# Performance work log

Measured on AMD Instinct MI355X. Metric: run time of the kernel, lower is better.

## Reference

```python
import jax, jax.numpy as jnp
import numpy as np

LEAK = 0.5  # LeakyReLU negative slope


def _binarize(w):
    # sign binarization with straight-through estimator (standard BinarizeConv2d /
    # CIM-sim quantized-weight behavior): forward uses sign(w) in {-1,+1},
    # backward passes gradient straight through.
    wb = jnp.where(w >= 0, 1.0, -1.0).astype(w.dtype)
    return w + jax.lax.stop_gradient(wb - w)


def _conv(x, w, b):
    # NCHW / OIHW, stride 1, no padding (matches nn.Conv2d(k, stride=1) defaults)
    y = jax.lax.conv_general_dilated(
        x, _binarize(w), window_strides=(1, 1), padding='VALID',
        dimension_numbers=('NCHW', 'OIHW', 'NCHW'))
    return y + b[None, :, None, None]


def _leaky(x):
    return jnp.where(x >= 0, x, LEAK * x)


def _maxpool2(x):
    # MaxPool2d(kernel_size=2), stride 2, floor mode == VALID reduce_window
    return jax.lax.reduce_window(x, -jnp.inf, jax.lax.max,
                                 (1, 1, 2, 2), (1, 1, 2, 2), 'VALID')


def setup_inputs() -> dict:
    key = jax.random.key(0)
    ks = jax.random.split(key, 9)
    f32 = jnp.float32
    return {
        'x':  jax.random.normal(ks[0], (32, 1, 224, 224), f32),
        'w1': jax.random.normal(ks[1], (128, 1, 3, 3), f32) * 0.1,
        'b1': jax.random.normal(ks[2], (128,), f32) * 0.1,
        'w2': jax.random.normal(ks[3], (64, 128, 3, 3), f32) * 0.1,
        'b2': jax.random.normal(ks[4], (64,), f32) * 0.1,
        'w3': jax.random.normal(ks[5], (32, 64, 3, 3), f32) * 0.1,
        'b3': jax.random.normal(ks[6], (32,), f32) * 0.1,
        'w4': jax.random.normal(ks[7], (8, 32, 3, 2), f32) * 0.1,
        'b4': jax.random.normal(ks[8], (8,), f32) * 0.1,
    }


def reference(x, w1, b1, w2, b2, w3, b3, w4, b4):
    x = _maxpool2(_leaky(_conv(x, w1, b1)))   # [B,128,111,111]
    x = _maxpool2(_leaky(_conv(x, w2, b2)))   # [B,64,54,54]
    x = _maxpool2(_leaky(_conv(x, w3, b3)))   # [B,32,26,26]
    x = _conv(x, w4, b4)                       # [B,8,24,25]
    return x.reshape(x.shape[0], -1)           # [B,4800]
```

## Files before the change

### kernel.cpp

```cpp
#include <hip/hip_runtime.h>
#include <hip/hip_bf16.h>

using bf16 = __hip_bfloat16;
typedef short  short8  __attribute__((ext_vector_type(8)));
typedef float  f32x4   __attribute__((ext_vector_type(4)));
typedef float  f32x16  __attribute__((ext_vector_type(16)));
typedef unsigned short us4 __attribute__((ext_vector_type(4)));

static __device__ __forceinline__ bf16  f2b(float v) { return __float2bfloat16(v); }
static __device__ __forceinline__ unsigned short f2bu(float v) {
    bf16 t = __float2bfloat16(v);
    return *(unsigned short*)&t;
}

__device__ __forceinline__ void pack32_one(const float* __restrict__ w,
                                           bf16* __restrict__ o, int i, int IC) {
    int j = i & 7;
    int l = (i >> 3) & 63;
    int f = i >> 9;
    int ICD16 = IC >> 4;
    int cc = f % ICD16;
    int t  = f / ICD16;
    int r  = t % 9;
    int mt = t / 9;
    int oc = mt * 32 + (l & 31);
    int ic = cc * 16 + ((l >> 5) << 3) + j;
    o[i] = f2b((w[(oc * IC + ic) * 9 + r] >= 0.f) ? 1.f : -1.f);
}

__global__ __launch_bounds__(256) void binpack_kernel(
    const float* __restrict__ w1, const float* __restrict__ w2,
    const float* __restrict__ w3, const float* __restrict__ w4,
    bf16* __restrict__ w1m, bf16* __restrict__ wA2,
    bf16* __restrict__ wA3, float* __restrict__ wc4) {
    int i = blockIdx.x * 256 + threadIdx.x;
    if (i < 73728) {
        pack32_one(w2, wA2, i, 128);
    } else if (i < 73728 + 18432) {
        pack32_one(w3, wA3, i - 73728, 64);
    } else if (i < 73728 + 18432 + 2048) {
        int k = i - (73728 + 18432);
        int j = k & 7, l = (k >> 3) & 63, mt = k >> 9;
        int ch = mt * 32 + (l & 31);
        int t = ((l >> 5) << 3) + j;
        w1m[k] = f2b(t < 9 ? ((w1[ch * 9 + t] >= 0.f) ? 1.f : -1.f) : 0.f);
    } else if (i < 73728 + 18432 + 2048 + 1536) {
        int k = i - (73728 + 18432 + 2048);
        int oc = k / 192, rem = k % 192;
        int ic = rem / 6, r = rem % 6;
        wc4[oc * 192 + r * 32 + ic] = (w4[k] >= 0.f) ? 1.f : -1.f;
    }
}

__global__ __launch_bounds__(256, 4) void conv1_kernel(
    const float* __restrict__ x, const bf16* __restrict__ w1m,
    const float* __restrict__ b1, bf16* __restrict__ a1) {
    __shared__ float xt[10][20];
    const int tid = threadIdx.x;
    const int b = blockIdx.z;
    const int pw0 = blockIdx.x * 8;
    const int ph0 = blockIdx.y * 4;
    const int r0 = ph0 * 2;
    const int c0 = pw0 * 2;

    if (tid < 180) {
        int row = tid / 18, col = tid - row * 18;
        int gr = r0 + row, gc = c0 + col;
        xt[row][col] = (gr < 224 && gc < 224)
                           ? x[((size_t)b * 224 + gr) * 224 + gc] : 0.f;
    }
    __syncthreads();

    const int w  = tid >> 6;
    const int l  = tid & 63;
    const int lc = l & 15;
    const int r2 = (l >> 4) & 1;
    const int hh = l >> 5;

    short8 af[4];
#pragma unroll
    for (int mt = 0; mt < 4; ++mt)
        af[mt] = ((const short8*)w1m)[mt * 64 + l];

    const int hl = 2 * w + r2;
    short8 bf;
    if (hh == 0) {
        bf[0] = (short)f2bu(xt[hl + 0][lc + 0]);
        bf[1] = (short)f2bu(xt[hl + 0][lc + 1]);
        bf[2] = (short)f2bu(xt[hl + 0][lc + 2]);
        bf[3] = (short)f2bu(xt[hl + 1][lc + 0]);
        bf[4] = (short)f2bu(xt[hl + 1][lc + 1]);
        bf[5] = (short)f2bu(xt[hl + 1][lc + 2]);
        bf[6] = (short)f2bu(xt[hl + 2][lc + 0]);
        bf[7] = (short)f2bu(xt[hl + 2][lc + 1]);
    } else {
        bf[0] = (short)f2bu(xt[hl + 2][lc + 2]);
        bf[1] = 0; bf[2] = 0; bf[3] = 0;
        bf[4] = 0; bf[5] = 0; bf[6] = 0; bf[7] = 0;
    }

    f32x16 acc[4];
#pragma unroll
    for (int mt = 0; mt < 4; ++mt) {
#pragma unroll
        for (int q = 0; q < 16; ++q) acc[mt][q] = 0.f;
        acc[mt] = __builtin_amdgcn_mfma_f32_32x32x16_bf16(af[mt], bf, acc[mt],
                                                          0, 0, 0);
    }

    const bool wr = ((l & 17) == 0);
    const int pw = pw0 + (lc >> 1);
    const int ph = ph0 + w;
    if (ph < 111 && pw < 111) {
#pragma unroll
        for (int mt = 0; mt < 4; ++mt) {
#pragma unroll
            for (int g = 0; g < 4; ++g) {
                f32x4 bias = *(const f32x4*)(b1 + mt * 32 + 8 * g + 4 * hh);
                us4 o;
#pragma unroll
                for (int q2 = 0; q2 < 4; ++q2) {
                    float v = acc[mt][g * 4 + q2] + bias[q2];
                    v = (v >= 0.f) ? v : 0.5f * v;
                    float m1 = fmaxf(v, __shfl_xor(v, 1));
                    float m  = fmaxf(m1, __shfl_xor(m1, 16));
                    o[q2] = f2bu(m);
                }
                if (wr)
                    *(us4*)(&a1[((size_t)(b * 111 + ph) * 111 + pw) * 128 +
                                mt * 32 + 8 * g + 4 * hh]) = o;
            }
        }
    }
}

template <int IC, int OC, int IN, int POOL>
__global__ __launch_bounds__(256, 4) void convmfma_kernel(
    const bf16* __restrict__ in, const bf16* __restrict__ wAp,
    const float* __restrict__ bias, bf16* __restrict__ out) {
    constexpr int MT = OC / 32;
    constexpr int CHUNKS = IC / 32;
    constexpr int ICD16 = IC / 16;
    __shared__ __align__(16) char smem[18 * 18 * 64];

    const int tid = threadIdx.x;
    const int b = blockIdx.z;
    const int oh0 = blockIdx.y * 16;
    const int ow0 = blockIdx.x * 16;

    const int w   = tid >> 6;
    const int l   = tid & 63;
    const int lc4 = l & 15;
    const int r2  = (l >> 4) & 1;
    const int hh  = l >> 5;

    f32x16 acc[MT][2];
#pragma unroll
    for (int mt = 0; mt < MT; ++mt)
#pragma unroll
        for (int nt = 0; nt < 2; ++nt)
#pragma unroll
            for (int q = 0; q < 16; ++q) acc[mt][nt][q] = 0.f;

    for (int chunk = 0; chunk < CHUNKS; ++chunk) {
        if (chunk) __syncthreads();
        {
            const bf16* src = in + ((size_t)b * IN * IN) * IC + chunk * 32;
            for (int u = tid; u < 18 * 18 * 4; u += 256) {
                int slot = u & 3, cell = u >> 2;
                int row = cell / 18, col = cell - row * 18;
                int gr = oh0 + row, gc = ow0 + col;
                f32x4 v = {0.f, 0.f, 0.f, 0.f};
                if (gr < IN && gc < IN)
                    v = *(const f32x4*)(src + ((size_t)gr * IN + gc) * IC + slot * 8);
                *(f32x4*)(smem + cell * 64 + ((slot ^ ((col >> 1) & 3)) << 4)) = v;
            }
        }
        __syncthreads();

#pragma unroll
        for (int kh = 0; kh < 3; ++kh) {
#pragma unroll
            for (int kw = 0; kw < 3; ++kw) {
                const int r = kh * 3 + kw;
                const int wincol = lc4 + kw;
                const int sx = (wincol >> 1) & 3;
#pragma unroll
                for (int cc = 0; cc < 2; ++cc) {
                    short8 af[MT];
#pragma unroll
                    for (int mt = 0; mt < MT; ++mt)
                        af[mt] = ((const short8*)wAp)[
                            (((mt * 9 + r) * ICD16) + chunk * 2 + cc) * 64 + l];
                    const int slot = cc * 2 + hh;
                    short8 bfr[2];
#pragma unroll
                    for (int nt = 0; nt < 2; ++nt) {
                        int cell = (4 * w + 2 * nt + r2 + kh) * 18 + wincol;
                        bfr[nt] = *(const short8*)(
                            smem + cell * 64 + ((slot ^ sx) << 4));
                    }
#pragma unroll
                    for (int mt = 0; mt < MT; ++mt)
#pragma unroll
                        for (int nt = 0; nt < 2; ++nt)
                            acc[mt][nt] = __builtin_amdgcn_mfma_f32_32x32x16_bf16(
                                af[mt], bfr[nt], acc[mt][nt], 0, 0, 0);
                }
            }
        }
    }

    const bool wr = ((l & 17) == 0);
    const int pw = blockIdx.x * 8 + (lc4 >> 1);
#pragma unroll
    for (int mt = 0; mt < MT; ++mt) {
#pragma unroll
        for (int nt = 0; nt < 2; ++nt) {
            const int ph = blockIdx.y * 8 + 2 * w + nt;
#pragma unroll
            for (int g = 0; g < 4; ++g) {
                us4 o;
#pragma unroll
                for (int q2 = 0; q2 < 4; ++q2) {
                    int q = g * 4 + q2;
                    int oc = mt * 32 + 8 * g + 4 * hh + q2;
                    float v = acc[mt][nt][q] + bias[oc];
                    v = (v >= 0.f) ? v : 0.5f * v;
                    float m1 = fmaxf(v, __shfl_xor(v, 1));
                    float m  = fmaxf(m1, __shfl_xor(m1, 16));
                    o[q2] = f2bu(m);
                }
                if (wr && ph < POOL && pw < POOL)
                    *(us4*)(&out[((size_t)(b * POOL + ph) * POOL + pw) * OC +
                                 mt * 32 + 8 * g + 4 * hh]) = o;
            }
        }
    }
}

__global__ __launch_bounds__(256) void conv4_kernel(
    const bf16* __restrict__ a3, const float* __restrict__ wc4,
    const float* __restrict__ b4, float* __restrict__ out) {
    int i = blockIdx.x * 256 + threadIdx.x;
    if (i >= 32 * 4800) return;
    int b = i / 4800;
    int rem = i % 4800;
    int oc = rem / 600;
    int r2 = rem % 600;
    int oh = r2 / 25, ow = r2 % 25;

    float acc = b4[oc];
    int rr = 0;
#pragma unroll
    for (int kh = 0; kh < 3; ++kh) {
#pragma unroll
        for (int kw = 0; kw < 2; ++kw, ++rr) {
            const bf16* xp = a3 + ((size_t)(b * 26 + oh + kh) * 26 + (ow + kw)) * 32;
            const float* wp = wc4 + oc * 192 + rr * 32;
            short8 x0 = *(const short8*)(xp);
            short8 x1 = *(const short8*)(xp + 8);
            short8 x2 = *(const short8*)(xp + 16);
            short8 x3 = *(const short8*)(xp + 24);
#pragma unroll
            for (int j = 0; j < 8; ++j) {
                union { short s; unsigned short u; } u0{x0[j]}, u1{x1[j]}, u2{x2[j]}, u3{x3[j]};
                acc += wp[j]      * __bfloat162float(__hip_bfloat16_raw{u0.u});
                acc += wp[8 + j]  * __bfloat162float(__hip_bfloat16_raw{u1.u});
                acc += wp[16 + j] * __bfloat162float(__hip_bfloat16_raw{u2.u});
                acc += wp[24 + j] * __bfloat162float(__hip_bfloat16_raw{u3.u});
            }
        }
    }
    out[i] = acc;
}

extern "C" void kernel_launch(void* const* d_in, const int* in_sizes, int n_in,
                              void* d_out, int out_size, void* d_ws, size_t ws_size,
                              hipStream_t stream) {
    const float* x  = (const float*)d_in[0];
    const float* w1 = (const float*)d_in[1];
    const float* b1 = (const float*)d_in[2];
    const float* w2 = (const float*)d_in[3];
    const float* b2 = (const float*)d_in[4];
    const float* w3 = (const float*)d_in[5];
    const float* b3 = (const float*)d_in[6];
    const float* w4 = (const float*)d_in[7];
    const float* b4 = (const float*)d_in[8];
    float* out = (float*)d_out;

    char* ws = (char*)d_ws;
    size_t off = 0;
    auto alloc = [&](size_t bytes) {
        void* p = ws + off;
        off = (off + bytes + 255) & ~(size_t)255;
        return p;
    };
    bf16* a1 = (bf16*)alloc((size_t)32 * 111 * 111 * 128 * 2);
    bf16* a2 = (bf16*)alloc((size_t)32 * 54 * 54 * 64 * 2);
    bf16* a3 = (bf16*)alloc((size_t)32 * 26 * 26 * 32 * 2);
    bf16* w1m = (bf16*)alloc(2048 * 2);
    bf16* wAp2 = (bf16*)alloc(73728 * 2);
    bf16* wAp3 = (bf16*)alloc(18432 * 2);
    float* wc4 = (float*)alloc(1536 * 4);

    binpack_kernel<<<dim3((95744 + 255) / 256), 256, 0, stream>>>(
        w1, w2, w3, w4, w1m, wAp2, wAp3, wc4);

    dim3 g1(14, 28, 32);
    conv1_kernel<<<g1, 256, 0, stream>>>(x, w1m, b1, a1);

    dim3 g2(7, 7, 32);
    convmfma_kernel<128, 64, 111, 54><<<g2, 256, 0, stream>>>(a1, wAp2, b2, a2);

    dim3 g3(4, 4, 32);
    convmfma_kernel<64, 32, 54, 26><<<g3, 256, 0, stream>>>(a2, wAp3, b3, a3);

    conv4_kernel<<<dim3((32 * 4800 + 255) / 256), 256, 0, stream>>>(
        a3, wc4, b4, out);
}
```

Baseline: 285.5 us.

## Retile MFMA conv to 8x32 output rows and reuse LDS B fragments across kh

Changes the conv2/conv3 MFMA tile from 16x16 to 8 rows by 32 columns, so each 32-wide MFMA N-dimension covers one output row. Four LDS rows are loaded once per (cc,kw) and reused across the three kh taps, cutting LDS reads. Max-pooling now takes the max of two accumulator rows in registers plus a single shuffle, and applies bias and LeakyReLU after the max, which is valid because both are monotonic. Launch bounds drop to 2 waves per EU, giving more registers but possibly lower occupancy, and the grids are resized to match.

```diff
diff --git a/kernel.cpp b/kernel.cpp
--- a/kernel.cpp
+++ b/kernel.cpp
@@ -135,24 +135,24 @@
 }
 
 template <int IC, int OC, int IN, int POOL>
-__global__ __launch_bounds__(256, 4) void convmfma_kernel(
+__global__ __launch_bounds__(256, 2) void convmfma_kernel(
     const bf16* __restrict__ in, const bf16* __restrict__ wAp,
     const float* __restrict__ bias, bf16* __restrict__ out) {
     constexpr int MT = OC / 32;
     constexpr int CHUNKS = IC / 32;
     constexpr int ICD16 = IC / 16;
-    __shared__ __align__(16) char smem[18 * 18 * 64];
+    constexpr int WROW = 10, WCOL = 34;
+    __shared__ __align__(16) char smem[WROW * WCOL * 64];
 
     const int tid = threadIdx.x;
     const int b = blockIdx.z;
-    const int oh0 = blockIdx.y * 16;
-    const int ow0 = blockIdx.x * 16;
-
-    const int w   = tid >> 6;
-    const int l   = tid & 63;
-    const int lc4 = l & 15;
-    const int r2  = (l >> 4) & 1;
-    const int hh  = l >> 5;
+    const int oh0 = blockIdx.y * 8;
+    const int ow0 = blockIdx.x * 32;
+
+    const int w  = tid >> 6;
+    const int l  = tid & 63;
+    const int n  = l & 31;
+    const int hh = l >> 5;
 
     f32x16 acc[MT][2];
 #pragma unroll
@@ -165,10 +165,10 @@
     for (int chunk = 0; chunk < CHUNKS; ++chunk) {
         if (chunk) __syncthreads();
         {
-            const bf16* src = in + ((size_t)b * IN * IN) * IC + chunk * 32;
-            for (int u = tid; u < 18 * 18 * 4; u += 256) {
+            const bf16* src = in + (size_t)b * IN * IN * IC + chunk * 32;
+            for (int u = tid; u < WROW * WCOL * 4; u += 256) {
                 int slot = u & 3, cell = u >> 2;
-                int row = cell / 18, col = cell - row * 18;
+                int row = cell / WCOL, col = cell - row * WCOL;
                 int gr = oh0 + row, gc = ow0 + col;
                 f32x4 v = {0.f, 0.f, 0.f, 0.f};
                 if (gr < IN && gc < IN)
@@ -179,62 +179,59 @@
         __syncthreads();
 
 #pragma unroll
-        for (int kh = 0; kh < 3; ++kh) {
+        for (int cc = 0; cc < 2; ++cc) {
 #pragma unroll
             for (int kw = 0; kw < 3; ++kw) {
-                const int r = kh * 3 + kw;
-                const int wincol = lc4 + kw;
+                const int wincol = n + kw;
                 const int sx = (wincol >> 1) & 3;
-#pragma unroll
-                for (int cc = 0; cc < 2; ++cc) {
+                const int slot = cc * 2 + hh;
+                short8 brow[4];
+#pragma unroll
+                for (int ar = 0; ar < 4; ++ar) {
+                    int cell = (2 * w + ar) * WCOL + wincol;
+                    brow[ar] = *(const short8*)(
+                        smem + cell * 64 + ((slot ^ sx) << 4));
+                }
+#pragma unroll
+                for (int kh = 0; kh < 3; ++kh) {
+                    const int r = kh * 3 + kw;
                     short8 af[MT];
 #pragma unroll
                     for (int mt = 0; mt < MT; ++mt)
                         af[mt] = ((const short8*)wAp)[
                             (((mt * 9 + r) * ICD16) + chunk * 2 + cc) * 64 + l];
-                    const int slot = cc * 2 + hh;
-                    short8 bfr[2];
-#pragma unroll
-                    for (int nt = 0; nt < 2; ++nt) {
-                        int cell = (4 * w + 2 * nt + r2 + kh) * 18 + wincol;
-                        bfr[nt] = *(const short8*)(
-                            smem + cell * 64 + ((slot ^ sx) << 4));
-                    }
-#pragma unroll
-                    for (int mt = 0; mt < MT; ++mt)
-#pragma unroll
-                        for (int nt = 0; nt < 2; ++nt)
+#pragma unroll
+                    for (int nt = 0; nt < 2; ++nt)
+#pragma unroll
+                        for (int mt = 0; mt < MT; ++mt)
                             acc[mt][nt] = __builtin_amdgcn_mfma_f32_32x32x16_bf16(
-                                af[mt], bfr[nt], acc[mt][nt], 0, 0, 0);
+                                af[mt], brow[nt + kh], acc[mt][nt], 0, 0, 0);
                 }
             }
         }
     }
 
-    const bool wr = ((l & 17) == 0);
-    const int pw = blockIdx.x * 8 + (lc4 >> 1);
+    const int pw = blockIdx.x * 16 + (n >> 1);
+    const int ph = blockIdx.y * 4 + w;
+    const bool wr = ((l & 1) == 0) && ph < POOL && pw < POOL;
 #pragma unroll
     for (int mt = 0; mt < MT; ++mt) {
 #pragma unroll
-        for (int nt = 0; nt < 2; ++nt) {
-            const int ph = blockIdx.y * 8 + 2 * w + nt;
-#pragma unroll
-            for (int g = 0; g < 4; ++g) {
-                us4 o;
-#pragma unroll
-                for (int q2 = 0; q2 < 4; ++q2) {
-                    int q = g * 4 + q2;
-                    int oc = mt * 32 + 8 * g + 4 * hh + q2;
-                    float v = acc[mt][nt][q] + bias[oc];
-                    v = (v >= 0.f) ? v : 0.5f * v;
-                    float m1 = fmaxf(v, __shfl_xor(v, 1));
-                    float m  = fmaxf(m1, __shfl_xor(m1, 16));
-                    o[q2] = f2bu(m);
-                }
-                if (wr && ph < POOL && pw < POOL)
-                    *(us4*)(&out[((size_t)(b * POOL + ph) * POOL + pw) * OC +
-                                 mt * 32 + 8 * g + 4 * hh]) = o;
-            }
+        for (int g = 0; g < 4; ++g) {
+            f32x4 bs = *(const f32x4*)(bias + mt * 32 + 8 * g + 4 * hh);
+            us4 o;
+#pragma unroll
+            for (int q2 = 0; q2 < 4; ++q2) {
+                int q = g * 4 + q2;
+                float v = fmaxf(acc[mt][0][q], acc[mt][1][q]);
+                v = fmaxf(v, __shfl_xor(v, 1));
+                v += bs[q2];
+                v = (v >= 0.f) ? v : 0.5f * v;
+                o[q2] = f2bu(v);
+            }
+            if (wr)
+                *(us4*)(&out[((size_t)(b * POOL + ph) * POOL + pw) * OC +
+                             mt * 32 + 8 * g + 4 * hh]) = o;
         }
     }
 }
@@ -310,10 +307,10 @@
     dim3 g1(14, 28, 32);
     conv1_kernel<<<g1, 256, 0, stream>>>(x, w1m, b1, a1);
 
-    dim3 g2(7, 7, 32);
+    dim3 g2(4, 14, 32);
     convmfma_kernel<128, 64, 111, 54><<<g2, 256, 0, stream>>>(a1, wAp2, b2, a2);
 
-    dim3 g3(4, 4, 32);
+    dim3 g3(2, 7, 32);
     convmfma_kernel<64, 32, 54, 26><<<g3, 256, 0, stream>>>(a2, wAp3, b3, a3);
 
     conv4_kernel<<<dim3((32 * 4800 + 255) / 256), 256, 0, stream>>>(
```

Result: faster. 258.0 us (-9.6%).
